# Kernel optimization log

Hardware: AMD Instinct MI355X
Metric: run time of the kernel (lower is better)

The kernel has to match this reference:

```python
import jax, jax.numpy as jnp
import numpy as np

DM = 1024        # model dim
E = 32           # totalexperts = expertsets*nexperts = 8*4
FE = 128         # expertsize
T = 4            # sparsity = nexperts (tokens per group)
EPS_TIEBREAK = 1e-6


def setup_inputs() -> dict:
    key = jax.random.key(0)
    k0, k1, k2, k3 = jax.random.split(key, 4)
    x = jax.random.normal(k0, (4, 4096, DM), dtype=jnp.float32)
    # fan_in-style inits matching misc.get_init_weight / get_init_bias
    controller = jax.random.normal(k1, (DM, E), dtype=jnp.float32) / np.float32(np.sqrt(DM))
    f1 = jax.random.normal(k2, (DM, E, FE), dtype=jnp.float32) / np.float32(np.sqrt(DM))
    bias = jnp.zeros((E, FE), dtype=jnp.float32)
    f2 = jax.random.normal(k3, (E, FE, DM), dtype=jnp.float32) / np.float32(np.sqrt(E * FE / T))
    return {"x": x, "controller": controller, "f1": f1, "bias": bias, "f2": f2}


def reference(x, controller, f1, bias, f2):
    B, S, d = x.shape
    t = T
    g = S // t
    # '... (b t) d -> ... b t d'
    grouped = x.reshape(B, g, t, d)
    # controller logits: '... t d, d e -> ... t e'
    logits = jnp.einsum('bgtd,de->bgte', grouped, controller)
    # deterministic tie-break offset over the t (slot) axis
    logits = logits + jnp.linspace(0.0, EPS_TIEBREAK, t, dtype=logits.dtype)[:, None]
    # softmax over dim=1 (group axis) as in original
    probs = jax.nn.softmax(logits, axis=1)
    # hard argmax mask over dim=-3 (group axis), scaled by soft probs
    perm = (logits == jnp.max(logits, axis=1, keepdims=True)).astype(x.dtype) * probs
    # expert up-projection with soft permutation: '... t d, d e f, ... t e -> ... e f'
    inner = jnp.einsum('bgtd,def,bgte->bgef', grouped, f1, perm)
    inner = jax.nn.relu(inner + bias)
    # expert down-projection: '... e f, e f d -> ... e d'
    inter = jnp.einsum('bgef,efd->bged', inner, f2)
    # unpermute: '... e d, ... t e -> ... t d'
    res = jnp.einsum('bged,bgte->bgtd', inter, perm)
    return res.reshape(B, S, d)
```

## Files before the change

kernel.cpp:

```cpp
#include <hip/hip_runtime.h>
#include <math.h>


#define DM   1024
#define NE   32
#define FE   128
#define T4   4
#define NB   4
#define SS   4096
#define NGRP 1024
#define NROW 512
#define LP_STRIDE (NROW * NGRP)

__global__ __launch_bounds__(256, 2)
void k_logits(const float* __restrict__ x, const float* __restrict__ ctrl,
              float* __restrict__ Lp, float* __restrict__ out)
{
    const int m      = blockIdx.x;
    const int ks     = blockIdx.y;
    const int tid    = threadIdx.x;
    const int base_s = m * 128;
    const int b      = base_s >> 12;
    const int g0     = (base_s & 4095) >> 2;

    __shared__ float xT[64 * 132];
    __shared__ float cs[64 * 32];

    const int tokg = tid & 31;
    const int eg   = tid >> 5;

    float acc[4][4];
#pragma unroll
    for (int i = 0; i < 4; ++i)
#pragma unroll
        for (int j = 0; j < 4; ++j) acc[i][j] = 0.f;

    const int row0 = tid >> 2;
    const int f4i  = tid & 3;

    for (int kit = 0; kit < 4; ++kit) {
        const int k0 = ks * 256 + kit * 64;
        __syncthreads();
#pragma unroll
        for (int rr = 0; rr < 2; ++rr) {
            const int row = row0 + rr * 64;
            const float* xp = x + (size_t)(base_s + row) * DM + k0;
#pragma unroll
            for (int cr = 0; cr < 4; ++cr) {
                const int col = f4i + cr * 4;
                const float4 v = *(const float4*)(xp + col * 4);
                const int d = col * 4;
                xT[(d + 0) * 132 + row] = v.x;
                xT[(d + 1) * 132 + row] = v.y;
                xT[(d + 2) * 132 + row] = v.z;
                xT[(d + 3) * 132 + row] = v.w;
            }
        }
        {
            const float4* cg = (const float4*)(ctrl + (size_t)k0 * NE);
            float4* cl = (float4*)cs;
            cl[tid]       = cg[tid];
            cl[tid + 256] = cg[tid + 256];
        }
        __syncthreads();
#pragma unroll 8
        for (int d = 0; d < 64; ++d) {
            const float4 xv = *(const float4*)(xT + d * 132 + tokg * 4);
            const float4 cv = *(const float4*)(cs + d * 32 + eg * 4);
            const float xa[4] = { xv.x, xv.y, xv.z, xv.w };
            const float ca[4] = { cv.x, cv.y, cv.z, cv.w };
#pragma unroll
            for (int i = 0; i < 4; ++i)
#pragma unroll
                for (int j = 0; j < 4; ++j) acc[i][j] += xa[i] * ca[j];
        }
    }

    {
        float* Lb = Lp + (size_t)ks * LP_STRIDE;
        const int g = g0 + tokg;
#pragma unroll
        for (int i = 0; i < 4; ++i)
#pragma unroll
            for (int j = 0; j < 4; ++j) {
                const int row = (b * T4 + i) * NE + eg * 4 + j;
                Lb[(size_t)row * NGRP + g] = acc[i][j];
            }
    }

    {
        const float4 z = make_float4(0.f, 0.f, 0.f, 0.f);
        float4* o4 = (float4*)(out + (size_t)(base_s + ks * 32) * DM);
#pragma unroll 4
        for (int i = tid; i < 32 * DM / 4; i += 256) o4[i] = z;
    }
}

__global__ __launch_bounds__(256, 1)
void k_expert(const float* __restrict__ x, const float* __restrict__ f1,
              const float* __restrict__ bias, const float* __restrict__ f2,
              const float* __restrict__ Lp, float* __restrict__ out)
{
    const int blk  = blockIdx.x;
    const int b    = blk >> 5;
    const int e    = blk & 31;
    const int tid  = threadIdx.x;
    const int lane = tid & 63;
    const int w    = tid >> 6;

    __shared__ float xr[T4][DM];
    __shared__ float wl[64 * FE];
    __shared__ float vv[T4][FE];
    __shared__ float hh[T4][FE];
    __shared__ int   gS[T4];
    __shared__ float pS[T4];

    {
        const int r = (b * T4 + w) * NE + e;
        const float* L0 = Lp + (size_t)r * NGRP;
        float mx = -INFINITY, s = 0.f;
        int gm = 0;
#pragma unroll
        for (int c = 0; c < 4; ++c) {
            const int g0c = c * 256 + lane * 4;
            const float4 v0 = *(const float4*)(L0 + g0c);
            const float4 v1 = *(const float4*)(L0 + 1 * LP_STRIDE + g0c);
            const float4 v2 = *(const float4*)(L0 + 2 * LP_STRIDE + g0c);
            const float4 v3 = *(const float4*)(L0 + 3 * LP_STRIDE + g0c);
            const float l[4] = { v0.x + v1.x + v2.x + v3.x,
                                 v0.y + v1.y + v2.y + v3.y,
                                 v0.z + v1.z + v2.z + v3.z,
                                 v0.w + v1.w + v2.w + v3.w };
#pragma unroll
            for (int j = 0; j < 4; ++j) {
                const float lv = l[j];
                if (lv > mx) { s = s * __expf(mx - lv) + 1.f; mx = lv; gm = g0c + j; }
                else         { s += __expf(lv - mx); }
            }
        }
#pragma unroll
        for (int off = 1; off < 64; off <<= 1) {
            const float m2 = __shfl_xor(mx, off);
            const float s2 = __shfl_xor(s, off);
            const int   g2 = __shfl_xor(gm, off);
            const float mn = fmaxf(mx, m2);
            s  = s * __expf(mx - mn) + s2 * __expf(m2 - mn);
            gm = (m2 > mx) ? g2 : ((m2 == mx && g2 < gm) ? g2 : gm);
            mx = mn;
        }
        if (lane == 0) { gS[w] = gm; pS[w] = 1.f / s; }
    }
    __syncthreads();

    int   gl[T4];
    float pl[T4];
#pragma unroll
    for (int t = 0; t < T4; ++t) { gl[t] = gS[t]; pl[t] = pS[t]; }

    {
        const float4* src = (const float4*)(x + ((size_t)b * SS + gl[w] * 4 + w) * DM);
        float4* dst = (float4*)xr[w];
        for (int i = lane; i < DM / 4; i += 64) dst[i] = src[i];
    }
    __syncthreads();

    {
        const int f    = tid & 127;
        const int half = tid >> 7;
        const float* x0 = xr[half * 2];
        const float* x1 = xr[half * 2 + 1];
        float a0 = 0.f, a1 = 0.f;
        for (int dc = 0; dc < 16; ++dc) {
            __syncthreads();
            {
                const int rr = tid >> 5, fq = tid & 31;
#pragma unroll
                for (int q = 0; q < 8; ++q) {
                    const int row = rr + q * 8;
                    const float4 v = *(const float4*)(f1 + (size_t)(dc * 64 + row) * (NE * FE)
                                                         + e * FE + fq * 4);
                    *(float4*)(wl + row * FE + fq * 4) = v;
                }
            }
            __syncthreads();
#pragma unroll 8
            for (int dl = 0; dl < 64; ++dl) {
                const float wv = wl[dl * FE + f];
                const int d = dc * 64 + dl;
                a0 += x0[d] * wv;
                a1 += x1[d] * wv;
            }
        }
        vv[half * 2][f]     = a0;
        vv[half * 2 + 1][f] = a1;
    }
    __syncthreads();

    if (tid < 128) {
        const int f = tid;
        const float bv = bias[e * FE + f];
#pragma unroll
        for (int t = 0; t < T4; ++t) {
            float u = bv;
#pragma unroll
            for (int t2 = 0; t2 < T4; ++t2)
                if (gl[t2] == gl[t]) u += pl[t2] * vv[t2][f];
            hh[t][f] = fmaxf(u, 0.f);
        }
    }
    __syncthreads();

    {
        const int d0 = tid * 4;
        float a[T4][4];
#pragma unroll
        for (int t = 0; t < T4; ++t)
#pragma unroll
            for (int j = 0; j < 4; ++j) a[t][j] = 0.f;

        const float* f2b = f2 + (size_t)e * FE * DM + d0;
#pragma unroll 4
        for (int f = 0; f < FE; ++f) {
            const float4 w4 = *(const float4*)(f2b + (size_t)f * DM);
#pragma unroll
            for (int t = 0; t < T4; ++t) {
                const float hv = hh[t][f];
                a[t][0] += hv * w4.x; a[t][1] += hv * w4.y;
                a[t][2] += hv * w4.z; a[t][3] += hv * w4.w;
            }
        }
#pragma unroll
        for (int t = 0; t < T4; ++t) {
            const float p = pl[t];
            float* orow = out + ((size_t)b * SS + gl[t] * 4 + t) * DM + d0;
            atomicAdd(orow + 0, p * a[t][0]);
            atomicAdd(orow + 1, p * a[t][1]);
            atomicAdd(orow + 2, p * a[t][2]);
            atomicAdd(orow + 3, p * a[t][3]);
        }
    }
}

extern "C" void kernel_launch(void* const* d_in, const int* in_sizes, int n_in,
                              void* d_out, int out_size, void* d_ws, size_t ws_size,
                              hipStream_t stream)
{
    const float* x    = (const float*)d_in[0];
    const float* ctrl = (const float*)d_in[1];
    const float* f1   = (const float*)d_in[2];
    const float* bias = (const float*)d_in[3];
    const float* f2   = (const float*)d_in[4];
    float* out = (float*)d_out;
    float* Lp  = (float*)d_ws;

    k_logits<<<dim3(128, 4), 256, 0, stream>>>(x, ctrl, Lp, out);
    k_expert<<<dim3(128), 256, 0, stream>>>(x, f1, bias, f2, Lp, out);
}
```

Before: 210.8 us.

## Split expert kernel into route, up and down kernels for more parallelism

The single 128-block expert kernel is replaced by three kernels. A routing kernel computes the argmax and softmax denominators. An up-projection kernel is split across 512 blocks by expert and 64-wide d chunk, and it batches all 4 batches' selected tokens so each f1 row is reused 16 times. A down-projection kernel over 256 blocks reduces the partial sums, applies bias and ReLU, and scatters through atomics. This exposes far more blocks to fill the GPU and reads each expert's weights once instead of once per batch, at the cost of extra launches and workspace round-trips.

```diff
diff --git a/kernel.cpp b/kernel.cpp
--- a/kernel.cpp
+++ b/kernel.cpp
@@ -6,11 +6,11 @@
 #define NE   32
 #define FE   128
 #define T4   4
-#define NB   4
 #define SS   4096
 #define NGRP 1024
 #define NROW 512
 #define LP_STRIDE (NROW * NGRP)
+#define VP_OFF   524288
 
 __global__ __launch_bounds__(256, 2)
 void k_logits(const float* __restrict__ x, const float* __restrict__ ctrl,
@@ -96,103 +96,131 @@
     }
 }
 
-__global__ __launch_bounds__(256, 1)
-void k_expert(const float* __restrict__ x, const float* __restrict__ f1,
-              const float* __restrict__ bias, const float* __restrict__ f2,
-              const float* __restrict__ Lp, float* __restrict__ out)
-{
-    const int blk  = blockIdx.x;
-    const int b    = blk >> 5;
-    const int e    = blk & 31;
-    const int tid  = threadIdx.x;
-    const int lane = tid & 63;
-    const int w    = tid >> 6;
-
-    __shared__ float xr[T4][DM];
-    __shared__ float wl[64 * FE];
-    __shared__ float vv[T4][FE];
-    __shared__ float hh[T4][FE];
-    __shared__ int   gS[T4];
-    __shared__ float pS[T4];
-
-    {
-        const int r = (b * T4 + w) * NE + e;
-        const float* L0 = Lp + (size_t)r * NGRP;
-        float mx = -INFINITY, s = 0.f;
-        int gm = 0;
-#pragma unroll
-        for (int c = 0; c < 4; ++c) {
-            const int g0c = c * 256 + lane * 4;
-            const float4 v0 = *(const float4*)(L0 + g0c);
-            const float4 v1 = *(const float4*)(L0 + 1 * LP_STRIDE + g0c);
-            const float4 v2 = *(const float4*)(L0 + 2 * LP_STRIDE + g0c);
-            const float4 v3 = *(const float4*)(L0 + 3 * LP_STRIDE + g0c);
-            const float l[4] = { v0.x + v1.x + v2.x + v3.x,
-                                 v0.y + v1.y + v2.y + v3.y,
-                                 v0.z + v1.z + v2.z + v3.z,
-                                 v0.w + v1.w + v2.w + v3.w };
-#pragma unroll
-            for (int j = 0; j < 4; ++j) {
-                const float lv = l[j];
-                if (lv > mx) { s = s * __expf(mx - lv) + 1.f; mx = lv; gm = g0c + j; }
-                else         { s += __expf(lv - mx); }
-            }
-        }
-#pragma unroll
-        for (int off = 1; off < 64; off <<= 1) {
-            const float m2 = __shfl_xor(mx, off);
-            const float s2 = __shfl_xor(s, off);
-            const int   g2 = __shfl_xor(gm, off);
-            const float mn = fmaxf(mx, m2);
-            s  = s * __expf(mx - mn) + s2 * __expf(m2 - mn);
-            gm = (m2 > mx) ? g2 : ((m2 == mx && g2 < gm) ? g2 : gm);
-            mx = mn;
-        }
-        if (lane == 0) { gS[w] = gm; pS[w] = 1.f / s; }
-    }
-    __syncthreads();
-
-    int   gl[T4];
-    float pl[T4];
-#pragma unroll
-    for (int t = 0; t < T4; ++t) { gl[t] = gS[t]; pl[t] = pS[t]; }
-
-    {
-        const float4* src = (const float4*)(x + ((size_t)b * SS + gl[w] * 4 + w) * DM);
-        float4* dst = (float4*)xr[w];
-        for (int i = lane; i < DM / 4; i += 64) dst[i] = src[i];
-    }
-    __syncthreads();
-
-    {
-        const int f    = tid & 127;
-        const int half = tid >> 7;
-        const float* x0 = xr[half * 2];
-        const float* x1 = xr[half * 2 + 1];
-        float a0 = 0.f, a1 = 0.f;
-        for (int dc = 0; dc < 16; ++dc) {
-            __syncthreads();
-            {
-                const int rr = tid >> 5, fq = tid & 31;
-#pragma unroll
-                for (int q = 0; q < 8; ++q) {
-                    const int row = rr + q * 8;
-                    const float4 v = *(const float4*)(f1 + (size_t)(dc * 64 + row) * (NE * FE)
-                                                         + e * FE + fq * 4);
-                    *(float4*)(wl + row * FE + fq * 4) = v;
-                }
-            }
-            __syncthreads();
+__global__ __launch_bounds__(128)
+void k_route(float* __restrict__ Lp)
+{
+    const int r    = blockIdx.x * 2 + (threadIdx.x >> 6);
+    const int lane = threadIdx.x & 63;
+    const float* L0 = Lp + (size_t)r * NGRP;
+
+    float mx = -INFINITY, s = 0.f;
+    int gm = 0;
+#pragma unroll
+    for (int c = 0; c < 4; ++c) {
+        const int g0c = c * 256 + lane * 4;
+        const float4 v0 = *(const float4*)(L0 + g0c);
+        const float4 v1 = *(const float4*)(L0 + 1 * LP_STRIDE + g0c);
+        const float4 v2 = *(const float4*)(L0 + 2 * LP_STRIDE + g0c);
+        const float4 v3 = *(const float4*)(L0 + 3 * LP_STRIDE + g0c);
+        const float l[4] = { v0.x + v1.x + v2.x + v3.x,
+                             v0.y + v1.y + v2.y + v3.y,
+                             v0.z + v1.z + v2.z + v3.z,
+                             v0.w + v1.w + v2.w + v3.w };
+#pragma unroll
+        for (int j = 0; j < 4; ++j) {
+            const float lv = l[j];
+            if (lv > mx) { s = s * __expf(mx - lv) + 1.f; mx = lv; gm = g0c + j; }
+            else         { s += __expf(lv - mx); }
+        }
+    }
+#pragma unroll
+    for (int off = 1; off < 64; off <<= 1) {
+        const float m2 = __shfl_xor(mx, off);
+        const float s2 = __shfl_xor(s, off);
+        const int   g2 = __shfl_xor(gm, off);
+        const float mn = fmaxf(mx, m2);
+        s  = s * __expf(mx - mn) + s2 * __expf(m2 - mn);
+        gm = (m2 > mx) ? g2 : ((m2 == mx && g2 < gm) ? g2 : gm);
+        mx = mn;
+    }
+    if (lane == 0) {
+        ((int*)Lp)[(size_t)r * NGRP] = gm;
+        Lp[(size_t)r * NGRP + 1] = 1.f / s;
+    }
+}
+
+__global__ __launch_bounds__(256, 2)
+void k_up(const float* __restrict__ x, const float* __restrict__ f1,
+          float* __restrict__ ws)
+{
+    const int e   = blockIdx.x & 31;
+    const int dc  = blockIdx.x >> 5;
+    const int tid = threadIdx.x;
+
+    __shared__ float xs[16 * 68];
+    __shared__ int   gS[16];
+
+    if (tid < 16) {
+        const int b = tid >> 2, t = tid & 3;
+        const int r = (b * T4 + t) * NE + e;
+        gS[tid] = ((const int*)ws)[(size_t)r * NGRP];
+    }
+    __syncthreads();
+
+    {
+        const int row = tid >> 4;
+        const int f4c = tid & 15;
+        const int b = row >> 2, t = row & 3;
+        const int s = b * SS + gS[row] * 4 + t;
+        const float4 v = *(const float4*)(x + (size_t)s * DM + dc * 64 + f4c * 4);
+        xs[row * 68 + f4c * 4 + 0] = v.x;
+        xs[row * 68 + f4c * 4 + 1] = v.y;
+        xs[row * 68 + f4c * 4 + 2] = v.z;
+        xs[row * 68 + f4c * 4 + 3] = v.w;
+    }
+    __syncthreads();
+
+    const int f4 = tid & 31;
+    const int rw = tid >> 5;
+    const float* f1p = f1 + (size_t)(dc * 64) * (NE * FE) + e * FE + f4 * 4;
+    const float* x0 = xs + (rw * 2) * 68;
+    const float* x1 = xs + (rw * 2 + 1) * 68;
+
+    float a0[4] = {0.f, 0.f, 0.f, 0.f}, a1[4] = {0.f, 0.f, 0.f, 0.f};
 #pragma unroll 8
-            for (int dl = 0; dl < 64; ++dl) {
-                const float wv = wl[dl * FE + f];
-                const int d = dc * 64 + dl;
-                a0 += x0[d] * wv;
-                a1 += x1[d] * wv;
-            }
-        }
-        vv[half * 2][f]     = a0;
-        vv[half * 2 + 1][f] = a1;
+    for (int dl = 0; dl < 64; ++dl) {
+        const float4 w4 = *(const float4*)(f1p + (size_t)dl * (NE * FE));
+        const float xa = x0[dl], xb = x1[dl];
+        a0[0] += xa * w4.x; a0[1] += xa * w4.y; a0[2] += xa * w4.z; a0[3] += xa * w4.w;
+        a1[0] += xb * w4.x; a1[1] += xb * w4.y; a1[2] += xb * w4.z; a1[3] += xb * w4.w;
+    }
+
+    float* Vp = ws + VP_OFF + (size_t)(dc * 32 + e) * (16 * FE);
+    *(float4*)(Vp + (rw * 2)     * FE + f4 * 4) = make_float4(a0[0], a0[1], a0[2], a0[3]);
+    *(float4*)(Vp + (rw * 2 + 1) * FE + f4 * 4) = make_float4(a1[0], a1[1], a1[2], a1[3]);
+}
+
+__global__ __launch_bounds__(256, 2)
+void k_down(const float* __restrict__ f2, const float* __restrict__ bias,
+            const float* __restrict__ ws, float* __restrict__ out)
+{
+    const int e   = blockIdx.x & 31;
+    const int dt  = blockIdx.x >> 5;
+    const int tid = threadIdx.x;
+
+    __shared__ float vv[16 * 132];
+    __shared__ float hh[16 * 132];
+    __shared__ int   gS[16];
+    __shared__ float pS[16];
+
+    if (tid < 16) {
+        const int b = tid >> 2, t = tid & 3;
+        const int r = (b * T4 + t) * NE + e;
+        gS[tid] = ((const int*)ws)[(size_t)r * NGRP];
+        pS[tid] = ws[(size_t)r * NGRP + 1];
+    }
+
+    {
+        const float* Vp = ws + VP_OFF;
+#pragma unroll
+        for (int q = 0; q < 8; ++q) {
+            const int i = tid + q * 256;
+            float s = 0.f;
+#pragma unroll
+            for (int dc = 0; dc < 16; ++dc)
+                s += Vp[(size_t)(dc * 32 + e) * (16 * FE) + i];
+            vv[(i >> 7) * 132 + (i & 127)] = s;
+        }
     }
     __syncthreads();
 
@@ -200,44 +228,51 @@
         const int f = tid;
         const float bv = bias[e * FE + f];
 #pragma unroll
-        for (int t = 0; t < T4; ++t) {
-            float u = bv;
-#pragma unroll
-            for (int t2 = 0; t2 < T4; ++t2)
-                if (gl[t2] == gl[t]) u += pl[t2] * vv[t2][f];
-            hh[t][f] = fmaxf(u, 0.f);
-        }
-    }
-    __syncthreads();
-
-    {
-        const int d0 = tid * 4;
-        float a[T4][4];
-#pragma unroll
-        for (int t = 0; t < T4; ++t)
-#pragma unroll
-            for (int j = 0; j < 4; ++j) a[t][j] = 0.f;
-
-        const float* f2b = f2 + (size_t)e * FE * DM + d0;
-#pragma unroll 4
-        for (int f = 0; f < FE; ++f) {
-            const float4 w4 = *(const float4*)(f2b + (size_t)f * DM);
+        for (int b = 0; b < 4; ++b) {
+            int   g[T4]; float p[T4], vl[T4];
 #pragma unroll
             for (int t = 0; t < T4; ++t) {
-                const float hv = hh[t][f];
-                a[t][0] += hv * w4.x; a[t][1] += hv * w4.y;
-                a[t][2] += hv * w4.z; a[t][3] += hv * w4.w;
-            }
-        }
-#pragma unroll
-        for (int t = 0; t < T4; ++t) {
-            const float p = pl[t];
-            float* orow = out + ((size_t)b * SS + gl[t] * 4 + t) * DM + d0;
-            atomicAdd(orow + 0, p * a[t][0]);
-            atomicAdd(orow + 1, p * a[t][1]);
-            atomicAdd(orow + 2, p * a[t][2]);
-            atomicAdd(orow + 3, p * a[t][3]);
-        }
+                g[t] = gS[b * 4 + t]; p[t] = pS[b * 4 + t];
+                vl[t] = vv[(b * 4 + t) * 132 + f];
+            }
+#pragma unroll
+            for (int t = 0; t < T4; ++t) {
+                float u = bv;
+#pragma unroll
+                for (int t2 = 0; t2 < T4; ++t2)
+                    if (g[t2] == g[t]) u += p[t2] * vl[t2];
+                hh[(b * 4 + t) * 132 + f] = fmaxf(u, 0.f);
+            }
+        }
+    }
+    __syncthreads();
+
+    const int d4 = tid & 31;
+    const int rw = tid >> 5;
+    const float* f2p = f2 + (size_t)e * FE * DM + dt * 128 + d4 * 4;
+    const float* h0 = hh + (rw * 2) * 132;
+    const float* h1 = hh + (rw * 2 + 1) * 132;
+
+    float a0[4] = {0.f, 0.f, 0.f, 0.f}, a1[4] = {0.f, 0.f, 0.f, 0.f};
+#pragma unroll 8
+    for (int f = 0; f < FE; ++f) {
+        const float4 w4 = *(const float4*)(f2p + (size_t)f * DM);
+        const float ha = h0[f], hb = h1[f];
+        a0[0] += ha * w4.x; a0[1] += ha * w4.y; a0[2] += ha * w4.z; a0[3] += ha * w4.w;
+        a1[0] += hb * w4.x; a1[1] += hb * w4.y; a1[2] += hb * w4.z; a1[3] += hb * w4.w;
+    }
+
+#pragma unroll
+    for (int h = 0; h < 2; ++h) {
+        const int row = rw * 2 + h;
+        const int b = row >> 2, t = row & 3;
+        const float p = pS[row];
+        const float* a = h ? a1 : a0;
+        float* orow = out + ((size_t)(b * SS + gS[row] * 4 + t)) * DM + dt * 128 + d4 * 4;
+        atomicAdd(orow + 0, p * a[0]);
+        atomicAdd(orow + 1, p * a[1]);
+        atomicAdd(orow + 2, p * a[2]);
+        atomicAdd(orow + 3, p * a[3]);
     }
 }
 
@@ -251,8 +286,10 @@
     const float* bias = (const float*)d_in[3];
     const float* f2   = (const float*)d_in[4];
     float* out = (float*)d_out;
-    float* Lp  = (float*)d_ws;
-
-    k_logits<<<dim3(128, 4), 256, 0, stream>>>(x, ctrl, Lp, out);
-    k_expert<<<dim3(128), 256, 0, stream>>>(x, f1, bias, f2, Lp, out);
-}
+    float* ws  = (float*)d_ws;
+
+    k_logits<<<dim3(128, 4), 256, 0, stream>>>(x, ctrl, ws, out);
+    k_route <<<dim3(256),    128, 0, stream>>>(ws);
+    k_up    <<<dim3(512),    256, 0, stream>>>(x, f1, ws);
+    k_down  <<<dim3(256),    256, 0, stream>>>(f2, bias, ws, out);
+}
```

Measured after the change: 199.9 us. 1.05x faster.
